# Kernel tuning notes

Hardware: AMD Instinct MI355X
Metric: run time of the kernel (lower is better)

The kernel has to match this reference:

```python
import jax, jax.numpy as jnp
import numpy as np

# AntModel forward, expressed at the ant-count level.
# Original: builds per-batch ragged routing tables where every ant at source
# neuron s is routed by the layer to a destination neuron; counts at each
# destination are accumulated, relu'd, and destinations with zero ants are
# pruned from the table (a no-op on the count vector itself). The deterministic
# layer routing used here is dest[s] = argmax(weights[s, :]).

B = 256
DIMS = [(4096, 4096), (4096, 4096), (4096, 1024)]
MAX_ANTS = 8


def setup_inputs() -> dict:
    key = jax.random.key(0)
    kx, k1, k2, k3 = jax.random.split(key, 4)
    x = jax.random.randint(kx, (B, DIMS[0][0]), 0, MAX_ANTS).astype(jnp.int32)
    W1 = jax.random.normal(k1, DIMS[0], dtype=jnp.float32)
    W2 = jax.random.normal(k2, DIMS[1], dtype=jnp.float32)
    W3 = jax.random.normal(k3, DIMS[2], dtype=jnp.float32)
    return {"x": x, "W1": W1, "W2": W2, "W3": W3}


def _layer(counts, W):
    # counts: [B, n_in] int32 ant counts; W: [n_in, n_out] pheromone weights
    dest = jnp.argmax(W, axis=1)  # [n_in] routing table
    n_out = W.shape[1]
    out = jnp.zeros((counts.shape[0], n_out), dtype=counts.dtype)
    out = out.at[:, dest].add(counts)  # scatter-add counts to destinations
    return jnp.maximum(out, 0)  # layer.relu_func (identity on counts)


def reference(x, W1, W2, W3):
    counts = x.astype(jnp.int32)
    for W in (W1, W2, W3):
        counts = _layer(counts, W)
    return counts.astype(jnp.float32)
```

## Files before the change

### kernel.cpp

```cpp
#include <hip/hip_runtime.h>


#define N_IN   4096
#define N_MID  4096
#define N_OUT  1024
#define BATCH  256

using u32 = unsigned int;
using u64 = unsigned long long;

__device__ __forceinline__ u32 forder(float f) {
    u32 b = __float_as_uint(f);
    return (b & 0x80000000u) ? ~b : (b | 0x80000000u);
}

__device__ __forceinline__ void upd(float v, int idx, float& bv, int& bi) {
    if (v > bv) { bv = v; bi = idx; }
}

__device__ __forceinline__ void wave_reduce(float& bv, int& bi) {
    #pragma unroll
    for (int off = 1; off < 64; off <<= 1) {
        float ov = __shfl_xor(bv, off, 64);
        int   oi = __shfl_xor(bi, off, 64);
        if (ov > bv || (ov == bv && oi < bi)) { bv = ov; bi = oi; }
    }
}

__global__ __launch_bounds__(256) void argmax_kernel(
    const float* __restrict__ W1, const float* __restrict__ W2,
    const float* __restrict__ W3, u64* __restrict__ p1,
    u64* __restrict__ p2, int* __restrict__ dest3) {
    const int g    = (blockIdx.x * 256 + (int)threadIdx.x) >> 6;
    const int lane = threadIdx.x & 63;

    if (g < 2 * (N_IN + N_MID)) {
        const bool  isW1 = g < 2 * N_IN;
        const int   idx  = g & (2 * N_IN - 1);
        const int   row  = idx >> 1;
        const int   half = idx & 1;
        const float4* __restrict__ p = reinterpret_cast<const float4*>(
            (isW1 ? W1 : W2) + (size_t)row * N_MID + half * 2048);
        float4 v[8];
        #pragma unroll
        for (int t = 0; t < 8; ++t) v[t] = p[t * 64 + lane];
        float bv = -__builtin_huge_valf(); int bi = 0;
        #pragma unroll
        for (int t = 0; t < 8; ++t) {
            const int c = half * 2048 + t * 256 + lane * 4;
            upd(v[t].x, c + 0, bv, bi);
            upd(v[t].y, c + 1, bv, bi);
            upd(v[t].z, c + 2, bv, bi);
            upd(v[t].w, c + 3, bv, bi);
        }
        wave_reduce(bv, bi);
        if (lane == 0) {
            u64 key = ((u64)forder(bv) << 32) | (u32)(~(u32)bi);
            atomicMax(&(isW1 ? p1 : p2)[row], key);
        }
    } else {
        const int r = g - 2 * (N_IN + N_MID);
        const float4* __restrict__ p =
            reinterpret_cast<const float4*>(W3 + (size_t)r * N_OUT);
        float4 v[4];
        #pragma unroll
        for (int t = 0; t < 4; ++t) v[t] = p[t * 64 + lane];
        float bv = -__builtin_huge_valf(); int bi = 0;
        #pragma unroll
        for (int t = 0; t < 4; ++t) {
            const int c = t * 256 + lane * 4;
            upd(v[t].x, c + 0, bv, bi);
            upd(v[t].y, c + 1, bv, bi);
            upd(v[t].z, c + 2, bv, bi);
            upd(v[t].w, c + 3, bv, bi);
        }
        wave_reduce(bv, bi);
        if (lane == 0) dest3[r] = bi;
    }
}

__global__ __launch_bounds__(256) void compose_kernel(
    const u64* __restrict__ p1, const u64* __restrict__ p2,
    const int* __restrict__ dest3, int* __restrict__ fdest) {
    const int s = blockIdx.x * blockDim.x + threadIdx.x;
    if (s < N_IN) {
        int d1 = (int)(~(u32)p1[s]) & (N_MID - 1);
        int d2 = (int)(~(u32)p2[d1]) & (N_MID - 1);
        fdest[s] = dest3[d2];
    }
}

__global__ __launch_bounds__(256) void scatter_kernel(
    const int* __restrict__ x, const int* __restrict__ fdest,
    float* __restrict__ out) {
    __shared__ int cnt[N_OUT];
    const int b = blockIdx.x;
    for (int i = threadIdx.x; i < N_OUT; i += 256) cnt[i] = 0;
    __syncthreads();
    const int4* __restrict__ x4 =
        reinterpret_cast<const int4*>(x + (size_t)b * N_IN);
    const int4* __restrict__ f4 = reinterpret_cast<const int4*>(fdest);
    for (int q = threadIdx.x; q < N_IN / 4; q += 256) {
        int4 v = x4[q];
        int4 d = f4[q];
        atomicAdd(&cnt[d.x], v.x);
        atomicAdd(&cnt[d.y], v.y);
        atomicAdd(&cnt[d.z], v.z);
        atomicAdd(&cnt[d.w], v.w);
    }
    __syncthreads();
    float* __restrict__ ob = out + (size_t)b * N_OUT;
    for (int i = threadIdx.x; i < N_OUT; i += 256) ob[i] = (float)cnt[i];
}

extern "C" void kernel_launch(void* const* d_in, const int* in_sizes, int n_in,
                              void* d_out, int out_size, void* d_ws, size_t ws_size,
                              hipStream_t stream) {
    const int*   x  = (const int*)d_in[0];
    const float* W1 = (const float*)d_in[1];
    const float* W2 = (const float*)d_in[2];
    const float* W3 = (const float*)d_in[3];
    float* out = (float*)d_out;

    u64* p1    = (u64*)d_ws;
    u64* p2    = p1 + N_IN;
    int* dest3 = (int*)(p2 + N_MID);
    int* fdest = dest3 + N_MID;

    hipMemsetAsync(p1, 0, 2 * N_IN * sizeof(u64), stream);

    const int total_waves = 2 * (N_IN + N_MID) + N_MID;
    argmax_kernel<<<total_waves / 4, 256, 0, stream>>>(W1, W2, W3, p1, p2,
                                                       dest3);
    compose_kernel<<<N_IN / 256, 256, 0, stream>>>(p1, p2, dest3, fdest);
    scatter_kernel<<<BATCH, 256, 0, stream>>>(x, fdest, out);
}
```

Before: 170.8 us.

## Skip argmax on W2 rows unreachable from W1 routing

Splits the combined argmax kernel so W1 and W3 are processed first. A small kernel then marks which middle neurons are reachable through W1's routing, and the W2 argmax is run only for those rows. This avoids reading W2 rows whose routing is never used. In exchange it adds two kernel launches and a serial dependency between the W1 and W2 passes.

```diff
diff --git a/kernel.cpp b/kernel.cpp
--- a/kernel.cpp
+++ b/kernel.cpp
@@ -27,39 +27,39 @@
     }
 }
 
-__global__ __launch_bounds__(256) void argmax_kernel(
-    const float* __restrict__ W1, const float* __restrict__ W2,
-    const float* __restrict__ W3, u64* __restrict__ p1,
-    u64* __restrict__ p2, int* __restrict__ dest3) {
+__device__ __forceinline__ void half_row_argmax(const float* __restrict__ W,
+                                                int row, int half, int lane,
+                                                u64* __restrict__ pk) {
+    const float4* __restrict__ p = reinterpret_cast<const float4*>(
+        W + (size_t)row * N_MID + half * 2048);
+    float4 v[8];
+    #pragma unroll
+    for (int t = 0; t < 8; ++t) v[t] = p[t * 64 + lane];
+    float bv = -__builtin_huge_valf(); int bi = 0;
+    #pragma unroll
+    for (int t = 0; t < 8; ++t) {
+        const int c = half * 2048 + t * 256 + lane * 4;
+        upd(v[t].x, c + 0, bv, bi);
+        upd(v[t].y, c + 1, bv, bi);
+        upd(v[t].z, c + 2, bv, bi);
+        upd(v[t].w, c + 3, bv, bi);
+    }
+    wave_reduce(bv, bi);
+    if (lane == 0) {
+        u64 key = ((u64)forder(bv) << 32) | (u32)(~(u32)bi);
+        atomicMax(&pk[row], key);
+    }
+}
+
+__global__ __launch_bounds__(256) void argmax_w1w3_kernel(
+    const float* __restrict__ W1, const float* __restrict__ W3,
+    u64* __restrict__ p1, int* __restrict__ dest3) {
     const int g    = (blockIdx.x * 256 + (int)threadIdx.x) >> 6;
     const int lane = threadIdx.x & 63;
-
-    if (g < 2 * (N_IN + N_MID)) {
-        const bool  isW1 = g < 2 * N_IN;
-        const int   idx  = g & (2 * N_IN - 1);
-        const int   row  = idx >> 1;
-        const int   half = idx & 1;
-        const float4* __restrict__ p = reinterpret_cast<const float4*>(
-            (isW1 ? W1 : W2) + (size_t)row * N_MID + half * 2048);
-        float4 v[8];
-        #pragma unroll
-        for (int t = 0; t < 8; ++t) v[t] = p[t * 64 + lane];
-        float bv = -__builtin_huge_valf(); int bi = 0;
-        #pragma unroll
-        for (int t = 0; t < 8; ++t) {
-            const int c = half * 2048 + t * 256 + lane * 4;
-            upd(v[t].x, c + 0, bv, bi);
-            upd(v[t].y, c + 1, bv, bi);
-            upd(v[t].z, c + 2, bv, bi);
-            upd(v[t].w, c + 3, bv, bi);
-        }
-        wave_reduce(bv, bi);
-        if (lane == 0) {
-            u64 key = ((u64)forder(bv) << 32) | (u32)(~(u32)bi);
-            atomicMax(&(isW1 ? p1 : p2)[row], key);
-        }
+    if (g < 2 * N_IN) {
+        half_row_argmax(W1, g >> 1, g & 1, lane, p1);
     } else {
-        const int r = g - 2 * (N_IN + N_MID);
+        const int r = g - 2 * N_IN;
         const float4* __restrict__ p =
             reinterpret_cast<const float4*>(W3 + (size_t)r * N_OUT);
         float4 v[4];
@@ -77,6 +77,25 @@
         wave_reduce(bv, bi);
         if (lane == 0) dest3[r] = bi;
     }
+}
+
+__global__ __launch_bounds__(256) void reach_kernel(
+    const u64* __restrict__ p1, int* __restrict__ reach2) {
+    const int s = blockIdx.x * 256 + threadIdx.x;
+    if (s < N_IN) {
+        int d1 = (int)(~(u32)p1[s]) & (N_MID - 1);
+        reach2[d1] = 1;
+    }
+}
+
+__global__ __launch_bounds__(256) void argmax_w2_kernel(
+    const float* __restrict__ W2, const int* __restrict__ reach2,
+    u64* __restrict__ p2) {
+    const int g    = (blockIdx.x * 256 + (int)threadIdx.x) >> 6;
+    const int lane = threadIdx.x & 63;
+    const int row  = g >> 1;
+    if (reach2[row] == 0) return;
+    half_row_argmax(W2, row, g & 1, lane, p2);
 }
 
 __global__ __launch_bounds__(256) void compose_kernel(
@@ -122,16 +141,19 @@
     const float* W3 = (const float*)d_in[3];
     float* out = (float*)d_out;
 
-    u64* p1    = (u64*)d_ws;
-    u64* p2    = p1 + N_IN;
-    int* dest3 = (int*)(p2 + N_MID);
-    int* fdest = dest3 + N_MID;
+    u64* p1     = (u64*)d_ws;
+    u64* p2     = p1 + N_IN;
+    int* reach2 = (int*)(p2 + N_MID);
+    int* dest3  = reach2 + N_MID;
+    int* fdest  = dest3 + N_MID;
 
-    hipMemsetAsync(p1, 0, 2 * N_IN * sizeof(u64), stream);
+    hipMemsetAsync(p1, 0, 2 * N_IN * sizeof(u64) + N_MID * sizeof(int),
+                   stream);
 
-    const int total_waves = 2 * (N_IN + N_MID) + N_MID;
-    argmax_kernel<<<total_waves / 4, 256, 0, stream>>>(W1, W2, W3, p1, p2,
-                                                       dest3);
+    argmax_w1w3_kernel<<<(2 * N_IN + N_MID) / 4, 256, 0, stream>>>(
+        W1, W3, p1, dest3);
+    reach_kernel<<<N_IN / 256, 256, 0, stream>>>(p1, reach2);
+    argmax_w2_kernel<<<(2 * N_MID) / 4, 256, 0, stream>>>(W2, reach2, p2);
     compose_kernel<<<N_IN / 256, 256, 0, stream>>>(p1, p2, dest3, fdest);
     scatter_kernel<<<BATCH, 256, 0, stream>>>(x, fdest, out);
 }
```

Measured after the change: 173.1 us. Within noise of the previous version (+1.3%).
